# Optimization experiments

Measured on AMD Instinct MI355X. Metric: run time of the kernel, lower is better.

## Reference

```python
import jax, jax.numpy as jnp
import numpy as np


def setup_inputs() -> dict:
    key = jax.random.key(0)
    k1, k2, k3 = jax.random.split(key, 3)
    B, K, IN, OUT = 4096, 8, 1024, 1024
    x = jax.random.normal(k1, (B, IN), dtype=jnp.float32)
    blend_weights = jax.random.uniform(k2, (B, K), dtype=jnp.float32)
    weight = jax.random.normal(k3, (K, OUT, IN), dtype=jnp.float32) * 0.01
    bias = jnp.zeros((K, OUT), dtype=jnp.float32)
    return {"x": x, "blend_weights": blend_weights, "weight": weight, "bias": bias}


def reference(x, blend_weights, weight, bias):
    # Mathematically identical to blending weights first then matvec:
    #   einsum('bk,koi->boi') then bmm  ==  per-expert GEMM then blend.
    # per-expert outputs: (b, k, o)
    expert_out = jnp.einsum('bi,koi->bko', x, weight)
    out = jnp.einsum('bk,bko->bo', blend_weights, expert_out)
    out = out + blend_weights @ bias  # (b,k) @ (k,o) -> (b,o)
    return out
```

## Files before the change

kernel.cpp:

```cpp
#include <hip/hip_runtime.h>
#include <hip/hip_bf16.h>
#include <stdint.h>

typedef short short8 __attribute__((ext_vector_type(8)));
typedef float f32x4  __attribute__((ext_vector_type(4)));
typedef unsigned short u16;

#define B_ROWS 4096
#define NEXP   8
#define IN_D   1024
#define OUT_D  1024

#define BM 128
#define BN 128
#define BK 64

__device__ __forceinline__ u16 f2bf(float f) {
    uint32_t u = __float_as_uint(f);
    uint32_t r = (u + 0x7fffu + ((u >> 16) & 1u)) >> 16;
    return (u16)r;
}

__global__ __launch_bounds__(256) void cvt_bf16(const float* __restrict__ in,
                                                u16* __restrict__ out, int n4) {
    int i = blockIdx.x * 256 + threadIdx.x;
    if (i >= n4) return;
    float4 v = reinterpret_cast<const float4*>(in)[i];
    ushort4 o;
    o.x = f2bf(v.x); o.y = f2bf(v.y); o.z = f2bf(v.z); o.w = f2bf(v.w);
    reinterpret_cast<ushort4*>(out)[i] = o;
}

__device__ __forceinline__ void glds16(const u16* g, u16* lds_base, int off_bytes) {
    auto gp = (const __attribute__((address_space(1))) void*)(uintptr_t)(g);
    auto lp = (__attribute__((address_space(3))) void*)(uintptr_t)((const char*)lds_base + off_bytes);
    __builtin_amdgcn_global_load_lds(gp, lp, 16, 0, 0);
}

__global__ __launch_bounds__(256, 2) void moe_gemm(
    const u16* __restrict__ Xb,
    const u16* __restrict__ Wb,
    const float* __restrict__ bwt,
    float* __restrict__ outp,
    int epb)
{
    __shared__ __align__(16) u16 As[BM * BK];
    __shared__ __align__(16) u16 Bs[BN * BK];

    const int tid  = threadIdx.x;
    const int lane = tid & 63, wid = tid >> 6;
    const int wm = wid >> 1, wn = wid & 1;
    const int lr = lane & 15, lg = lane >> 4;
    const int bn = blockIdx.x * BN;
    const int bm = blockIdx.y * BM;
    const int bz = blockIdx.z;

    int st_row[4], st_col[4], st_off[4];
    #pragma unroll
    for (int r = 0; r < 4; ++r) {
        int c = r * 256 + wid * 64 + lane;
        st_row[r] = c >> 3;
        st_col[r] = (c & 7) * 8;
        st_off[r] = (r * 256 + wid * 64) * 16;
    }

    f32x4 acc_t[4][4];
    #pragma unroll
    for (int mi = 0; mi < 4; ++mi)
        #pragma unroll
        for (int ni = 0; ni < 4; ++ni)
            acc_t[mi][ni] = (f32x4){0.f, 0.f, 0.f, 0.f};

    const int nsteps = IN_D / BK;
    for (int e = 0; e < epb; ++e) {
        const int kexp = bz * epb + e;
        const u16* Wk = Wb + (size_t)kexp * OUT_D * IN_D;

        f32x4 acc_e[4][4];
        #pragma unroll
        for (int mi = 0; mi < 4; ++mi)
            #pragma unroll
            for (int ni = 0; ni < 4; ++ni)
                acc_e[mi][ni] = (f32x4){0.f, 0.f, 0.f, 0.f};

        for (int it = 0; it < nsteps; ++it) {
            const int i0 = it * BK;
            __syncthreads();
            #pragma unroll
            for (int r = 0; r < 4; ++r) {
                glds16(Xb + (size_t)(bm + st_row[r]) * IN_D + i0 + st_col[r], As, st_off[r]);
                glds16(Wk + (size_t)(bn + st_row[r]) * IN_D + i0 + st_col[r], Bs, st_off[r]);
            }
            __syncthreads();

            #pragma unroll
            for (int ks = 0; ks < 2; ++ks) {
                short8 a[4], b[4];
                #pragma unroll
                for (int mi = 0; mi < 4; ++mi)
                    a[mi] = *(const short8*)(As + (wm * 64 + mi * 16 + lr) * BK + ks * 32 + lg * 8);
                #pragma unroll
                for (int ni = 0; ni < 4; ++ni)
                    b[ni] = *(const short8*)(Bs + (wn * 64 + ni * 16 + lr) * BK + ks * 32 + lg * 8);
                #pragma unroll
                for (int mi = 0; mi < 4; ++mi)
                    #pragma unroll
                    for (int ni = 0; ni < 4; ++ni)
                        acc_e[mi][ni] = __builtin_amdgcn_mfma_f32_16x16x32_bf16(
                            a[mi], b[ni], acc_e[mi][ni], 0, 0, 0);
            }
        }

        #pragma unroll
        for (int mi = 0; mi < 4; ++mi) {
            #pragma unroll
            for (int r = 0; r < 4; ++r) {
                const int grow = bm + wm * 64 + mi * 16 + lg * 4 + r;
                const float w = bwt[grow * NEXP + kexp];
                #pragma unroll
                for (int ni = 0; ni < 4; ++ni)
                    acc_t[mi][ni][r] += w * acc_e[mi][ni][r];
            }
        }
    }

    float* op = outp + (size_t)bz * B_ROWS * OUT_D;
    #pragma unroll
    for (int mi = 0; mi < 4; ++mi)
        #pragma unroll
        for (int ni = 0; ni < 4; ++ni)
            #pragma unroll
            for (int r = 0; r < 4; ++r) {
                const int grow = bm + wm * 64 + mi * 16 + lg * 4 + r;
                const int gcol = bn + wn * 64 + ni * 16 + lr;
                op[(size_t)grow * OUT_D + gcol] = acc_t[mi][ni][r];
            }
}

__global__ __launch_bounds__(256) void reduce_bias(
    const float* __restrict__ parts, const float* __restrict__ bwt,
    const float* __restrict__ bias, float* __restrict__ out, int nz)
{
    const int i4 = blockIdx.x * 256 + threadIdx.x;
    const size_t total = (size_t)B_ROWS * OUT_D;
    const size_t base = (size_t)i4 * 4;
    if (base >= total) return;
    const int brow = (int)(base >> 10);
    const int o = (int)(base & 1023);

    float4 s;
    if (nz == 0) s = *reinterpret_cast<const float4*>(out + base);
    else         s = make_float4(0.f, 0.f, 0.f, 0.f);
    for (int z = 0; z < nz; ++z) {
        float4 p = *reinterpret_cast<const float4*>(parts + (size_t)z * total + base);
        s.x += p.x; s.y += p.y; s.z += p.z; s.w += p.w;
    }
    #pragma unroll
    for (int k = 0; k < NEXP; ++k) {
        const float w = bwt[brow * NEXP + k];
        float4 bb = *reinterpret_cast<const float4*>(bias + k * OUT_D + o);
        s.x += w * bb.x; s.y += w * bb.y; s.z += w * bb.z; s.w += w * bb.w;
    }
    *reinterpret_cast<float4*>(out + base) = s;
}

__global__ __launch_bounds__(256) void naive_moe(
    const float* __restrict__ x, const float* __restrict__ bwt,
    const float* __restrict__ wgt, const float* __restrict__ bias,
    float* __restrict__ out)
{
    __shared__ float xs[IN_D];
    const int brow = blockIdx.x;
    const int o = blockIdx.y * 256 + threadIdx.x;
    for (int i = threadIdx.x; i < IN_D; i += 256) xs[i] = x[(size_t)brow * IN_D + i];
    __syncthreads();
    float acc = 0.f;
    for (int k = 0; k < NEXP; ++k) {
        const float* wr = wgt + ((size_t)k * OUT_D + o) * IN_D;
        float d = 0.f;
        for (int i = 0; i < IN_D; ++i) d += xs[i] * wr[i];
        acc += bwt[brow * NEXP + k] * (d + bias[k * OUT_D + o]);
    }
    out[(size_t)brow * OUT_D + o] = acc;
}

extern "C" void kernel_launch(void* const* d_in, const int* in_sizes, int n_in,
                              void* d_out, int out_size, void* d_ws, size_t ws_size,
                              hipStream_t stream) {
    const float* x    = (const float*)d_in[0];
    const float* bwt  = (const float*)d_in[1];
    const float* wgt  = (const float*)d_in[2];
    const float* bias = (const float*)d_in[3];
    float* out = (float*)d_out;

    const size_t xb_bytes   = (size_t)B_ROWS * IN_D * 2;
    const size_t wb_bytes   = (size_t)NEXP * OUT_D * IN_D * 2;
    const size_t part_bytes = (size_t)B_ROWS * OUT_D * 4;
    const size_t base_bytes = xb_bytes + wb_bytes;

    if (ws_size < base_bytes) {
        naive_moe<<<dim3(B_ROWS, OUT_D / 256), 256, 0, stream>>>(x, bwt, wgt, bias, out);
        return;
    }

    int nz = 1;
    if      (ws_size >= base_bytes + 4 * part_bytes) nz = 4;
    else if (ws_size >= base_bytes + 2 * part_bytes) nz = 2;
    const bool have_part = ws_size >= base_bytes + (size_t)nz * part_bytes;

    u16* xb = (u16*)d_ws;
    u16* wb = (u16*)((char*)d_ws + xb_bytes);
    float* parts = (float*)((char*)d_ws + base_bytes);

    cvt_bf16<<<(B_ROWS * IN_D / 4 + 255) / 256, 256, 0, stream>>>(x, xb, B_ROWS * IN_D / 4);
    cvt_bf16<<<(NEXP * OUT_D * IN_D / 4 + 255) / 256, 256, 0, stream>>>(wgt, wb, NEXP * OUT_D * IN_D / 4);

    float* gout = have_part ? parts : out;
    moe_gemm<<<dim3(OUT_D / BN, B_ROWS / BM, nz), 256, 0, stream>>>(xb, wb, bwt, gout, NEXP / nz);

    reduce_bias<<<((B_ROWS * OUT_D / 4) + 255) / 256, 256, 0, stream>>>(
        have_part ? parts : nullptr, bwt, bias, out, have_part ? nz : 0);
}
```

Before: 215.7 us.

## Pre-scale activations by blend weights so experts accumulate into one accumulator

A new prep kernel builds eight bf16 copies of x, each scaled by that row's blend weight for one expert. The GEMM can then chain every expert's K-loop into a single accumulator, with no per-expert epilogue and no second register tile. Split-K over experts drops from up to 4 partitions to 2, with one partition written straight to out, which cuts partial-buffer traffic. The cost is a much larger A operand read from memory (8x the bf16 x, about 64MB), extra bf16 rounding of the scaled products, and launch bounds that no longer guarantee 2 waves.

```diff
diff --git a/kernel.cpp b/kernel.cpp
--- a/kernel.cpp
+++ b/kernel.cpp
@@ -19,6 +19,24 @@
     uint32_t u = __float_as_uint(f);
     uint32_t r = (u + 0x7fffu + ((u >> 16) & 1u)) >> 16;
     return (u16)r;
+}
+
+__global__ __launch_bounds__(256) void build_a(const float* __restrict__ x,
+                                               const float* __restrict__ bwt,
+                                               u16* __restrict__ a) {
+    const int t = blockIdx.x * 256 + threadIdx.x;
+    const int b = t >> 8, i4 = t & 255;
+    float4 v = reinterpret_cast<const float4*>(x)[(size_t)b * 256 + i4];
+    float4 w0 = reinterpret_cast<const float4*>(bwt)[b * 2];
+    float4 w1 = reinterpret_cast<const float4*>(bwt)[b * 2 + 1];
+    float wk[8] = {w0.x, w0.y, w0.z, w0.w, w1.x, w1.y, w1.z, w1.w};
+    #pragma unroll
+    for (int k = 0; k < NEXP; ++k) {
+        ushort4 o;
+        o.x = f2bf(wk[k] * v.x); o.y = f2bf(wk[k] * v.y);
+        o.z = f2bf(wk[k] * v.z); o.w = f2bf(wk[k] * v.w);
+        reinterpret_cast<ushort4*>(a)[((size_t)k * B_ROWS + b) * 256 + i4] = o;
+    }
 }
 
 __global__ __launch_bounds__(256) void cvt_bf16(const float* __restrict__ in,
@@ -37,11 +55,11 @@
     __builtin_amdgcn_global_load_lds(gp, lp, 16, 0, 0);
 }
 
-__global__ __launch_bounds__(256, 2) void moe_gemm(
-    const u16* __restrict__ Xb,
+__global__ __launch_bounds__(256) void moe_gemm(
+    const u16* __restrict__ Ab,
     const u16* __restrict__ Wb,
-    const float* __restrict__ bwt,
-    float* __restrict__ outp,
+    float* __restrict__ out0,
+    float* __restrict__ out1,
     int epb)
 {
     __shared__ __align__(16) u16 As[BM * BK];
@@ -64,31 +82,25 @@
         st_off[r] = (r * 256 + wid * 64) * 16;
     }
 
-    f32x4 acc_t[4][4];
+    f32x4 acc[4][4];
     #pragma unroll
     for (int mi = 0; mi < 4; ++mi)
         #pragma unroll
         for (int ni = 0; ni < 4; ++ni)
-            acc_t[mi][ni] = (f32x4){0.f, 0.f, 0.f, 0.f};
+            acc[mi][ni] = (f32x4){0.f, 0.f, 0.f, 0.f};
 
     const int nsteps = IN_D / BK;
     for (int e = 0; e < epb; ++e) {
         const int kexp = bz * epb + e;
+        const u16* Ak = Ab + (size_t)kexp * B_ROWS * IN_D;
         const u16* Wk = Wb + (size_t)kexp * OUT_D * IN_D;
-
-        f32x4 acc_e[4][4];
-        #pragma unroll
-        for (int mi = 0; mi < 4; ++mi)
-            #pragma unroll
-            for (int ni = 0; ni < 4; ++ni)
-                acc_e[mi][ni] = (f32x4){0.f, 0.f, 0.f, 0.f};
 
         for (int it = 0; it < nsteps; ++it) {
             const int i0 = it * BK;
             __syncthreads();
             #pragma unroll
             for (int r = 0; r < 4; ++r) {
-                glds16(Xb + (size_t)(bm + st_row[r]) * IN_D + i0 + st_col[r], As, st_off[r]);
+                glds16(Ak + (size_t)(bm + st_row[r]) * IN_D + i0 + st_col[r], As, st_off[r]);
                 glds16(Wk + (size_t)(bn + st_row[r]) * IN_D + i0 + st_col[r], Bs, st_off[r]);
             }
             __syncthreads();
@@ -106,25 +118,13 @@
                 for (int mi = 0; mi < 4; ++mi)
                     #pragma unroll
                     for (int ni = 0; ni < 4; ++ni)
-                        acc_e[mi][ni] = __builtin_amdgcn_mfma_f32_16x16x32_bf16(
-                            a[mi], b[ni], acc_e[mi][ni], 0, 0, 0);
+                        acc[mi][ni] = __builtin_amdgcn_mfma_f32_16x16x32_bf16(
+                            a[mi], b[ni], acc[mi][ni], 0, 0, 0);
             }
         }
-
-        #pragma unroll
-        for (int mi = 0; mi < 4; ++mi) {
-            #pragma unroll
-            for (int r = 0; r < 4; ++r) {
-                const int grow = bm + wm * 64 + mi * 16 + lg * 4 + r;
-                const float w = bwt[grow * NEXP + kexp];
-                #pragma unroll
-                for (int ni = 0; ni < 4; ++ni)
-                    acc_t[mi][ni][r] += w * acc_e[mi][ni][r];
-            }
-        }
-    }
-
-    float* op = outp + (size_t)bz * B_ROWS * OUT_D;
+    }
+
+    float* op = (bz == 0) ? out0 : out1;
     #pragma unroll
     for (int mi = 0; mi < 4; ++mi)
         #pragma unroll
@@ -133,13 +133,13 @@
             for (int r = 0; r < 4; ++r) {
                 const int grow = bm + wm * 64 + mi * 16 + lg * 4 + r;
                 const int gcol = bn + wn * 64 + ni * 16 + lr;
-                op[(size_t)grow * OUT_D + gcol] = acc_t[mi][ni][r];
+                op[(size_t)grow * OUT_D + gcol] = acc[mi][ni][r];
             }
 }
 
 __global__ __launch_bounds__(256) void reduce_bias(
     const float* __restrict__ parts, const float* __restrict__ bwt,
-    const float* __restrict__ bias, float* __restrict__ out, int nz)
+    const float* __restrict__ bias, float* __restrict__ out, int np)
 {
     const int i4 = blockIdx.x * 256 + threadIdx.x;
     const size_t total = (size_t)B_ROWS * OUT_D;
@@ -148,10 +148,8 @@
     const int brow = (int)(base >> 10);
     const int o = (int)(base & 1023);
 
-    float4 s;
-    if (nz == 0) s = *reinterpret_cast<const float4*>(out + base);
-    else         s = make_float4(0.f, 0.f, 0.f, 0.f);
-    for (int z = 0; z < nz; ++z) {
+    float4 s = *reinterpret_cast<const float4*>(out + base);
+    for (int z = 0; z < np; ++z) {
         float4 p = *reinterpret_cast<const float4*>(parts + (size_t)z * total + base);
         s.x += p.x; s.y += p.y; s.z += p.z; s.w += p.w;
     }
@@ -193,31 +191,30 @@
     const float* bias = (const float*)d_in[3];
     float* out = (float*)d_out;
 
-    const size_t xb_bytes   = (size_t)B_ROWS * IN_D * 2;
-    const size_t wb_bytes   = (size_t)NEXP * OUT_D * IN_D * 2;
+    const size_t a_bytes    = (size_t)NEXP * B_ROWS * IN_D * 2;
+    const size_t w_bytes    = (size_t)NEXP * OUT_D * IN_D * 2;
     const size_t part_bytes = (size_t)B_ROWS * OUT_D * 4;
-    const size_t base_bytes = xb_bytes + wb_bytes;
-
-    if (ws_size < base_bytes) {
+
+    if (ws_size < a_bytes + w_bytes) {
         naive_moe<<<dim3(B_ROWS, OUT_D / 256), 256, 0, stream>>>(x, bwt, wgt, bias, out);
         return;
     }
 
-    int nz = 1;
-    if      (ws_size >= base_bytes + 4 * part_bytes) nz = 4;
-    else if (ws_size >= base_bytes + 2 * part_bytes) nz = 2;
-    const bool have_part = ws_size >= base_bytes + (size_t)nz * part_bytes;
-
-    u16* xb = (u16*)d_ws;
-    u16* wb = (u16*)((char*)d_ws + xb_bytes);
-    float* parts = (float*)((char*)d_ws + base_bytes);
-
-    cvt_bf16<<<(B_ROWS * IN_D / 4 + 255) / 256, 256, 0, stream>>>(x, xb, B_ROWS * IN_D / 4);
-    cvt_bf16<<<(NEXP * OUT_D * IN_D / 4 + 255) / 256, 256, 0, stream>>>(wgt, wb, NEXP * OUT_D * IN_D / 4);
-
-    float* gout = have_part ? parts : out;
-    moe_gemm<<<dim3(OUT_D / BN, B_ROWS / BM, nz), 256, 0, stream>>>(xb, wb, bwt, gout, NEXP / nz);
-
-    reduce_bias<<<((B_ROWS * OUT_D / 4) + 255) / 256, 256, 0, stream>>>(
-        have_part ? parts : nullptr, bwt, bias, out, have_part ? nz : 0);
-}
+    u16* ab = (u16*)d_ws;
+    u16* wb = (u16*)((char*)d_ws + a_bytes);
+    float* parts = (float*)((char*)d_ws + a_bytes + w_bytes);
+
+    const int nz = (ws_size >= a_bytes + w_bytes + part_bytes) ? 2 : 1;
+
+    build_a<<<B_ROWS, 256, 0, stream>>>(x, bwt, ab);
+    cvt_bf16<<<(NEXP * OUT_D * IN_D / 4 + 255) / 256, 256, 0, stream>>>(
+        wgt, wb, NEXP * OUT_D * IN_D / 4);
+
+    if (nz == 2) {
+        moe_gemm<<<dim3(OUT_D / BN, B_ROWS / BM, 2), 256, 0, stream>>>(ab, wb, parts, out, NEXP / 2);
+        reduce_bias<<<((B_ROWS * OUT_D / 4) + 255) / 256, 256, 0, stream>>>(parts, bwt, bias, out, 1);
+    } else {
+        moe_gemm<<<dim3(OUT_D / BN, B_ROWS / BM, 1), 256, 0, stream>>>(ab, wb, out, out, NEXP);
+        reduce_bias<<<((B_ROWS * OUT_D / 4) + 255) / 256, 256, 0, stream>>>(nullptr, bwt, bias, out, 0);
+    }
+}
```

After: 205.7 us. 1.05x faster.
